# Optimization experiments

Hardware: AMD Instinct MI355X
Metric: run time of the kernel (lower is better)

## Reference

```python
import jax, jax.numpy as jnp
import numpy as np
import math


def _alibi_slopes(n_heads):
    def pow2_slopes(n):
        start = 2.0 ** (-2.0 ** (-(math.log2(n) - 3)))
        return [start * start ** i for i in range(n)]
    if math.log2(n_heads) % 1 == 0:
        return np.array(pow2_slopes(n_heads), dtype=np.float32)
    closest = 2 ** math.floor(math.log2(n_heads))
    base = pow2_slopes(closest)
    extra = pow2_slopes(2 * closest)[0::2][: n_heads - closest]
    return np.array(base + extra, dtype=np.float32)


def setup_inputs() -> dict:
    key = jax.random.key(0)
    ks = jax.random.split(key, 5)
    B, T, D = 2, 2048, 1024
    scale = 1.0 / math.sqrt(D)
    return {
        "x": jax.random.normal(ks[0], (B, T, D), dtype=jnp.float32),
        "Wq": jax.random.normal(ks[1], (D, D), dtype=jnp.float32) * scale,
        "Wk": jax.random.normal(ks[2], (D, D), dtype=jnp.float32) * scale,
        "Wv": jax.random.normal(ks[3], (D, D), dtype=jnp.float32) * scale,
        "Wo": jax.random.normal(ks[4], (D, D), dtype=jnp.float32) * scale,
        "window": 256,
    }


def reference(x, Wq, Wk, Wv, Wo, window):
    B, T, D = x.shape
    H = 16
    d_k = D // H

    def proj(W):
        # torch nn.Linear: y = x @ W.T ; then (B,T,H,dk) -> (B,H,T,dk)
        return (x @ W.T).reshape(B, T, H, d_k).transpose(0, 2, 1, 3)

    Q, K, V = proj(Wq), proj(Wk), proj(Wv)
    scores = jnp.einsum("bhtk,bhsk->bhts", Q, K) / math.sqrt(d_k)

    pos = jnp.arange(T)
    dist = jnp.abs(pos[None, :] - pos[:, None]).astype(jnp.float32)  # (T,T)
    slopes = jnp.asarray(_alibi_slopes(H))  # (H,)
    alibi = -slopes[:, None, None] * dist  # (H,T,T)
    win_mask = jnp.where(dist > window // 2, -jnp.inf, 0.0)  # (T,T)

    scores = scores + alibi[None] + win_mask[None, None]
    attn = jax.nn.softmax(scores, axis=-1)  # dropout=0.0 (eval)
    out = jnp.einsum("bhts,bhsd->bthd", attn, V).reshape(B, T, D)
    return out @ Wo.T, attn
```

## Files before the change

kernel.cpp:

```cpp
#include <hip/hip_runtime.h>
#include <hip/hip_bf16.h>


typedef __bf16 bf16x8 __attribute__((ext_vector_type(8)));
typedef float f32x4 __attribute__((ext_vector_type(4)));

__device__ __forceinline__ float bf2f(unsigned short u) {
    union { unsigned int i; float f; } v; v.i = ((unsigned int)u) << 16; return v.f;
}
__device__ __forceinline__ unsigned short f2bf(float f) {
    union { float f; unsigned int i; } v; v.f = f;
    unsigned int r = v.i + 0x7FFFu + ((v.i >> 16) & 1u);
    return (unsigned short)(r >> 16);
}

__global__ __launch_bounds__(256) void cast_all(
    const float* __restrict__ x,
    const float* __restrict__ wq, const float* __restrict__ wk,
    const float* __restrict__ wv, const float* __restrict__ wo,
    unsigned short* __restrict__ xb, unsigned short* __restrict__ wb)
{
    const int slice = blockIdx.y;
    const int i = (blockIdx.x * 256 + threadIdx.x) * 4;
    const float* src;
    unsigned short* dst;
    if (slice < 4) {
        src = x + (size_t)slice * 1048576;
        dst = xb + (size_t)slice * 1048576;
    } else {
        const float* ws4[4] = {wq, wk, wv, wo};
        src = ws4[slice - 4];
        dst = wb + (size_t)(slice - 4) * 1048576;
    }
    const float4 v = *(const float4*)(src + i);
    ushort4 o;
    o.x = f2bf(v.x); o.y = f2bf(v.y); o.z = f2bf(v.z); o.w = f2bf(v.w);
    *(ushort4*)(dst + i) = o;
}

#define GLDS16(g, l) __builtin_amdgcn_global_load_lds(                      \
    (const __attribute__((address_space(1))) void*)(g),                     \
    (__attribute__((address_space(3))) void*)(l), 16, 0, 0)

__global__ __launch_bounds__(256) void gemm_bf16_nt(
    const unsigned short* __restrict__ A, const unsigned short* __restrict__ Bm,
    unsigned short* __restrict__ qkv, int M, int N, int K)
{
    __shared__ __align__(16) unsigned short As[128 * 32];
    __shared__ __align__(16) unsigned short Bs[128 * 32];
    __shared__ __align__(16) unsigned short Cs[64][136];

    const int tid  = threadIdx.x;
    const int lane = tid & 63, w = tid >> 6;

    const int lin = (int)(blockIdx.y * gridDim.x + blockIdx.x);
    const int swz = (lin & 7) * 96 + (lin >> 3);
    const int bx = swz % 24, by = swz / 24;
    const int bm = by * 128, bn = bx * 128;

    const unsigned short* ga = A  + (size_t)(bm + w * 16 + (lane >> 2)) * K + (lane & 3) * 8;
    const unsigned short* gb = Bm + (size_t)(bn + w * 16 + (lane >> 2)) * K + (lane & 3) * 8;
    unsigned short* laA0 = &As[w * 512];
    unsigned short* laA1 = &As[2048 + w * 512];
    unsigned short* laB0 = &Bs[w * 512];
    unsigned short* laB1 = &Bs[2048 + w * 512];

    const int wr = w >> 1, wc = w & 1;
    const int fr = lane & 15, fq = lane >> 4;

    f32x4 acc[4][4] = {};

    for (int k0 = 0; k0 < K; k0 += 32) {
        GLDS16(ga + k0, laA0);
        GLDS16(ga + k0 + (size_t)64 * K, laA1);
        GLDS16(gb + k0, laB0);
        GLDS16(gb + k0 + (size_t)64 * K, laB1);
        __syncthreads();
        bf16x8 af[4], bfv[4];
#pragma unroll
        for (int i = 0; i < 4; ++i)
            af[i] = *(const bf16x8*)&As[(wr * 64 + i * 16 + fr) * 32 + fq * 8];
#pragma unroll
        for (int j = 0; j < 4; ++j)
            bfv[j] = *(const bf16x8*)&Bs[(wc * 64 + j * 16 + fr) * 32 + fq * 8];
#pragma unroll
        for (int i = 0; i < 4; ++i)
#pragma unroll
            for (int j = 0; j < 4; ++j)
                acc[i][j] = __builtin_amdgcn_mfma_f32_16x16x32_bf16(af[i], bfv[j], acc[i][j], 0, 0, 0);
        __syncthreads();
    }

    const int which = bn >> 10;
#pragma unroll
    for (int half = 0; half < 2; ++half) {
        __syncthreads();
        if (which == 2) {
            if (wc == half) {
#pragma unroll
                for (int i = 0; i < 4; ++i)
#pragma unroll
                    for (int j = 0; j < 4; ++j) {
                        const int lr = wr * 64 + i * 16 + fq * 4;
                        const int lc = j * 16 + fr;
#pragma unroll
                        for (int r = 0; r < 4; ++r)
                            Cs[lc][lr + r] = f2bf(acc[i][j][r]);
                    }
            }
        } else {
            if (wr == half) {
#pragma unroll
                for (int i = 0; i < 4; ++i)
#pragma unroll
                    for (int j = 0; j < 4; ++j) {
                        const int lr = i * 16 + fq * 4;
                        const int lc = wc * 64 + j * 16 + fr;
#pragma unroll
                        for (int r = 0; r < 4; ++r)
                            Cs[lr + r][lc] = f2bf(acc[i][j][r]);
                    }
            }
        }
        __syncthreads();
#pragma unroll
        for (int rep = 0; rep < 4; ++rep) {
            const int idx = rep * 256 + tid;
            const int row = idx >> 4;
            const int ch  = idx & 15;
            const bf16x8 vv = *(const bf16x8*)&Cs[row][ch * 8];
            if (which == 2) {
                const int nn = bn + half * 64 + row;
                const int hh = (nn >> 6) & 15, dd = nn & 63;
                const int mm = bm + ch * 8;
                const int bb = mm >> 11, tt = mm & 2047;
                *(bf16x8*)(qkv + (size_t)2 * 4194304 +
                           (((size_t)bb * 16 + hh) * 64 + dd) * 2048 + tt) = vv;
            } else {
                const int mm = bm + half * 64 + row;
                const int bb = mm >> 11, tt = mm & 2047;
                const int nn = bn + ch * 8;
                const int hh = (nn >> 6) & 15, dd = nn & 63;
                *(bf16x8*)(qkv + (size_t)which * 4194304 +
                           (((size_t)bb * 16 + hh) * 2048 + tt) * 64 + dd) = vv;
            }
        }
    }
}

__global__ __launch_bounds__(256) void gemm_bf16_nt_out(
    const unsigned short* __restrict__ A, const unsigned short* __restrict__ Bm,
    float* __restrict__ C, int M, int N, int K)
{
    __shared__ __align__(16) unsigned short As[64 * 32];
    __shared__ __align__(16) unsigned short Bs[128 * 32];

    const int tid  = threadIdx.x;
    const int lane = tid & 63, w = tid >> 6;

    const int lin = (int)(blockIdx.y * gridDim.x + blockIdx.x);
    const int swz = (lin & 7) * 64 + (lin >> 3);
    const int bx = swz & 7, by = swz >> 3;
    const int bm = by * 64, bn = bx * 128;

    const unsigned short* ga = A  + (size_t)(bm + w * 16 + (lane >> 2)) * K + (lane & 3) * 8;
    const unsigned short* gb = Bm + (size_t)(bn + w * 16 + (lane >> 2)) * K + (lane & 3) * 8;
    unsigned short* laA  = &As[w * 512];
    unsigned short* laB0 = &Bs[w * 512];
    unsigned short* laB1 = &Bs[2048 + w * 512];

    const int wr = w >> 1, wc = w & 1;
    const int fr = lane & 15, fq = lane >> 4;

    f32x4 acc[2][4] = {};

    for (int k0 = 0; k0 < K; k0 += 32) {
        GLDS16(ga + k0, laA);
        GLDS16(gb + k0, laB0);
        GLDS16(gb + k0 + (size_t)64 * K, laB1);
        __syncthreads();
        bf16x8 af[2], bfv[4];
#pragma unroll
        for (int i = 0; i < 2; ++i)
            af[i] = *(const bf16x8*)&As[(wr * 32 + i * 16 + fr) * 32 + fq * 8];
#pragma unroll
        for (int j = 0; j < 4; ++j)
            bfv[j] = *(const bf16x8*)&Bs[(wc * 64 + j * 16 + fr) * 32 + fq * 8];
#pragma unroll
        for (int i = 0; i < 2; ++i)
#pragma unroll
            for (int j = 0; j < 4; ++j)
                acc[i][j] = __builtin_amdgcn_mfma_f32_16x16x32_bf16(af[i], bfv[j], acc[i][j], 0, 0, 0);
        __syncthreads();
    }

#pragma unroll
    for (int i = 0; i < 2; ++i)
#pragma unroll
        for (int j = 0; j < 4; ++j) {
            const int mb = bm + wr * 32 + i * 16 + fq * 4;
            const int n  = bn + wc * 64 + j * 16 + fr;
#pragma unroll
            for (int r = 0; r < 4; ++r)
                __builtin_nontemporal_store(acc[i][j][r], &C[(size_t)(mb + r) * N + n]);
        }
}

#define NT_MAX 20
__global__ __launch_bounds__(256) void attn_mfma(
    const unsigned short* __restrict__ Q, const unsigned short* __restrict__ K,
    const unsigned short* __restrict__ VT, float* __restrict__ attn,
    unsigned short* __restrict__ ao, const int* __restrict__ wptr)
{
    const int T = 2048;
    __shared__ __align__(16) unsigned short Plds[4][16][328];

    const int bid = (int)blockIdx.x;
    const int swz = (bid & 7) * 128 + (bid >> 3);
    const int w = threadIdx.x >> 6, lane = threadIdx.x & 63;
    const int fr = lane & 15, fq = lane >> 4;

    const int tblk = swz & 31;
    const int h    = (swz >> 5) & 15;
    const int b    = swz >> 9;
    const int t0   = tblk * 64;

    const int W2 = wptr[0] >> 1;
    const int sA = (t0 - W2) > 0 ? (t0 - W2) : 0;
    int sB = t0 + 63 + W2; if (sB > T - 1) sB = T - 1;
    const int sEnd = sB + 1;
    const int nt  = (sEnd - sA) >> 4;
    const int ncc = (nt + 1) >> 1;

    const size_t bhT = ((size_t)b * 16 + h) * T;
    const unsigned short* Qbh  = Q  + bhT * 64;
    const unsigned short* Kbh  = K  + bhT * 64;
    const unsigned short* VTbh = VT + (((size_t)b * 16 + h) * 64) * T;

    bf16x8 aq0 = *(const bf16x8*)(Qbh + (size_t)(t0 + w * 16 + fr) * 64 + fq * 8);
    bf16x8 aq1 = *(const bf16x8*)(Qbh + (size_t)(t0 + w * 16 + fr) * 64 + 32 + fq * 8);

    const float slope = exp2f(-0.5f * (float)(h + 1));
    const int trow0 = t0 + w * 16 + fq * 4;

    f32x4 sc[NT_MAX];
#pragma unroll
    for (int st = 0; st < NT_MAX; ++st) {
        const int sbase = sA + st * 16;
        if (sbase < sEnd) {
            const unsigned short* kb = Kbh + (size_t)(sbase + fr) * 64 + fq * 8;
            bf16x8 b0 = *(const bf16x8*)(kb);
            bf16x8 b1 = *(const bf16x8*)(kb + 32);
            f32x4 sv = {0.f, 0.f, 0.f, 0.f};
            sv = __builtin_amdgcn_mfma_f32_16x16x32_bf16(aq0, b0, sv, 0, 0, 0);
            sv = __builtin_amdgcn_mfma_f32_16x16x32_bf16(aq1, b1, sv, 0, 0, 0);
            const int scol = sbase + fr;
#pragma unroll
            for (int rr = 0; rr < 4; ++rr) {
                const int d = trow0 + rr - scol;
                const int ad = d < 0 ? -d : d;
                const float val = sv[rr] * 0.125f - slope * (float)ad;
                sc[st][rr] = (ad <= W2) ? val : -1e30f;
            }
        } else {
            sc[st] = (f32x4){-1e30f, -1e30f, -1e30f, -1e30f};
        }
    }

    {
        const f32x4 z4 = {0.f, 0.f, 0.f, 0.f};
        for (int i = 0; i < 16; ++i) {
            float* row = attn + (bhT + t0 + w * 16 + i) * T;
            for (int c = lane * 4; c < sA; c += 256)
                __builtin_nontemporal_store(z4, (f32x4*)(row + c));
            for (int c = sEnd + lane * 4; c < T; c += 256)
                __builtin_nontemporal_store(z4, (f32x4*)(row + c));
        }
    }

    float inv[4];
#pragma unroll
    for (int rr = 0; rr < 4; ++rr) {
        float m = -1e30f;
#pragma unroll
        for (int st = 0; st < NT_MAX; ++st) m = fmaxf(m, sc[st][rr]);
#pragma unroll
        for (int off = 1; off < 16; off <<= 1) m = fmaxf(m, __shfl_xor(m, off, 64));
        float s = 0.f;
#pragma unroll
        for (int st = 0; st < NT_MAX; ++st) {
            const float p = __expf(sc[st][rr] - m);
            sc[st][rr] = p;
            s += p;
        }
#pragma unroll
        for (int off = 1; off < 16; off <<= 1) s += __shfl_xor(s, off, 64);
        inv[rr] = 1.0f / s;
    }

#pragma unroll
    for (int st = 0; st < NT_MAX; ++st) {
        const int sbase = sA + st * 16;
        if (sbase < sEnd) {
#pragma unroll
            for (int rr = 0; rr < 4; ++rr)
                Plds[w][fq * 4 + rr][st * 16 + fr] = f2bf(sc[st][rr] * inv[rr]);
        } else {
#pragma unroll
            for (int rr = 0; rr < 4; ++rr)
                Plds[w][fq * 4 + rr][st * 16 + fr] = 0;
        }
    }

    for (int i = 0; i < 16; ++i) {
        float* row = attn + (bhT + t0 + w * 16 + i) * T;
        const unsigned short* prow = &Plds[w][i][0];
#pragma unroll
        for (int jj = 0; jj < 2; ++jj) {
            const int pc = (jj * 64 + lane) * 4;
            const int c = sA + pc;
            if (c < sEnd) {
                const ushort4 p4 = *(const ushort4*)(prow + pc);
                f32x4 v;
                v[0] = bf2f(p4.x);
                v[1] = bf2f(p4.y);
                v[2] = bf2f(p4.z);
                v[3] = bf2f(p4.w);
                __builtin_nontemporal_store(v, (f32x4*)(row + c));
            }
        }
    }

    f32x4 oacc[4] = {};
    bf16x8 vt[4], vtn[4];
#pragma unroll
    for (int j = 0; j < 4; ++j)
        vt[j] = *(const bf16x8*)(VTbh + (size_t)(j * 16 + fr) * T + sA + fq * 8);
    for (int c = 0; c < ncc; ++c) {
        const bf16x8 pa = *(const bf16x8*)&Plds[w][fr][c * 32 + fq * 8];
        if (c + 1 < ncc) {
#pragma unroll
            for (int j = 0; j < 4; ++j)
                vtn[j] = *(const bf16x8*)(VTbh + (size_t)(j * 16 + fr) * T + sA + (c + 1) * 32 + fq * 8);
        }
#pragma unroll
        for (int j = 0; j < 4; ++j)
            oacc[j] = __builtin_amdgcn_mfma_f32_16x16x32_bf16(pa, vt[j], oacc[j], 0, 0, 0);
#pragma unroll
        for (int j = 0; j < 4; ++j) vt[j] = vtn[j];
    }

#pragma unroll
    for (int j = 0; j < 4; ++j)
#pragma unroll
        for (int rr = 0; rr < 4; ++rr)
            Plds[w][fq * 4 + rr][j * 16 + fr] = f2bf(oacc[j][rr]);
#pragma unroll
    for (int s = 0; s < 2; ++s) {
        const int idx = s * 64 + lane;
        const int row = idx >> 3;
        const int ch  = idx & 7;
        const bf16x8 vv = *(const bf16x8*)&Plds[w][row][ch * 8];
        *(bf16x8*)(ao + ((size_t)b * T + t0 + w * 16 + row) * 1024 + h * 64 + ch * 8) = vv;
    }
}

extern "C" void kernel_launch(void* const* d_in, const int* in_sizes, int n_in,
                              void* d_out, int out_size, void* d_ws, size_t ws_size,
                              hipStream_t stream)
{
    const float* x  = (const float*)d_in[0];
    const float* Wq = (const float*)d_in[1];
    const float* Wk = (const float*)d_in[2];
    const float* Wv = (const float*)d_in[3];
    const float* Wo = (const float*)d_in[4];
    const int*  win = (const int*)d_in[5];

    const int M = 4096, D = 1024;

    unsigned short* xb    = (unsigned short*)d_ws;
    unsigned short* Wqkvb = xb + (size_t)M * D;
    unsigned short* Wob   = Wqkvb + (size_t)3 * D * D;
    unsigned short* QKVb  = Wob + (size_t)D * D;
    unsigned short* AOb   = QKVb + (size_t)3 * M * D;

    float* out  = (float*)d_out;
    float* attn = out + (size_t)M * D;

    {
        dim3 g(1024, 8);
        cast_all<<<g, 256, 0, stream>>>(x, Wq, Wk, Wv, Wo, xb, Wqkvb);
    }

    {
        dim3 g(3072 / 128, M / 128);
        gemm_bf16_nt<<<g, 256, 0, stream>>>(xb, Wqkvb, QKVb, M, 3072, D);
    }

    attn_mfma<<<1024, 256, 0, stream>>>(
        QKVb, QKVb + (size_t)M * D, QKVb + (size_t)2 * M * D, attn, AOb, win);

    {
        dim3 g(D / 128, M / 64);
        gemm_bf16_nt_out<<<g, 256, 0, stream>>>(AOb, Wob, out, M, D, D);
    }
}
```

Baseline: 197.7 us.

## Fold batch-0 attention zero-fill into QKV GEMM launch as extra blocks

After: 201.3 us. Within noise of the previous version (+1.8%).

```diff
diff --git a/kernel.cpp b/kernel.cpp
--- a/kernel.cpp
+++ b/kernel.cpp
@@ -42,18 +42,39 @@
     (const __attribute__((address_space(1))) void*)(g),                     \
     (__attribute__((address_space(3))) void*)(l), 16, 0, 0)
 
-__global__ __launch_bounds__(256) void gemm_bf16_nt(
+__global__ __launch_bounds__(256) void gemm_qkv_fill(
     const unsigned short* __restrict__ A, const unsigned short* __restrict__ Bm,
-    unsigned short* __restrict__ qkv, int M, int N, int K)
+    unsigned short* __restrict__ qkv, float* __restrict__ attnbuf,
+    const int* __restrict__ wptr, int M, int N, int K)
 {
-    __shared__ __align__(16) unsigned short As[128 * 32];
-    __shared__ __align__(16) unsigned short Bs[128 * 32];
-    __shared__ __align__(16) unsigned short Cs[64][136];
-
+    __shared__ __align__(16) unsigned char smem[17408];
+    unsigned short* As = (unsigned short*)smem;
+    unsigned short* Bs = As + 4096;
+    typedef unsigned short CsRow[136];
+    CsRow* Cs = (CsRow*)smem;
+
+    const int lin = (int)blockIdx.x;
     const int tid  = threadIdx.x;
     const int lane = tid & 63, w = tid >> 6;
 
-    const int lin = (int)(blockIdx.y * gridDim.x + blockIdx.x);
+    if (lin >= 768) {
+        const int slab = lin - 768;
+        const int W2f = wptr[0] >> 1;
+        const int t0f = (slab & 31) * 64;
+        const int sAf = (t0f - W2f) > 0 ? (t0f - W2f) : 0;
+        int sEf = t0f + 64 + W2f; if (sEf > 2048) sEf = 2048;
+        const size_t rowbase = (size_t)((slab >> 5) & 15) * 2048 + t0f;
+        const f32x4 z4 = {0.f, 0.f, 0.f, 0.f};
+        for (int i = 0; i < 16; ++i) {
+            float* rp = attnbuf + (rowbase + w * 16 + i) * 2048;
+            for (int c = lane * 4; c < sAf; c += 256)
+                __builtin_nontemporal_store(z4, (f32x4*)(rp + c));
+            for (int c = sEf + lane * 4; c < 2048; c += 256)
+                __builtin_nontemporal_store(z4, (f32x4*)(rp + c));
+        }
+        return;
+    }
+
     const int swz = (lin & 7) * 96 + (lin >> 3);
     const int bx = swz % 24, by = swz / 24;
     const int bm = by * 128, bn = bx * 128;
@@ -267,7 +288,7 @@
         }
     }
 
-    {
+    if (b) {
         const f32x4 z4 = {0.f, 0.f, 0.f, 0.f};
         for (int i = 0; i < 16; ++i) {
             float* row = attn + (bhT + t0 + w * 16 + i) * T;
@@ -392,10 +413,8 @@
         cast_all<<<g, 256, 0, stream>>>(x, Wq, Wk, Wv, Wo, xb, Wqkvb);
     }
 
-    {
-        dim3 g(3072 / 128, M / 128);
-        gemm_bf16_nt<<<g, 256, 0, stream>>>(xb, Wqkvb, QKVb, M, 3072, D);
-    }
+    gemm_qkv_fill<<<1280, 256, 0, stream>>>(xb, Wqkvb, QKVb, attn, win,
+                                            M, 3072, D);
 
     attn_mfma<<<1024, 256, 0, stream>>>(
         QKVb, QKVb + (size_t)M * D, QKVb + (size_t)2 * M * D, attn, AOb, win);
```
